# Performance work log

Measured on AMD Instinct MI355X. Metric: run time of the kernel, lower is better.

Reference implementation:

```python
import jax, jax.numpy as jnp
import numpy as np

B, H, L, TAU, THETA = 8192, 256, 4, 8, 8


def setup_inputs() -> dict:
    key = jax.random.key(0)
    ks = jax.random.split(key, 16)
    w = lambda k, shape: (jax.random.normal(k, shape, jnp.float32) * 0.02)
    return {
        "x": jax.random.normal(ks[0], (B, H), jnp.float32),
        "t_att": jax.random.normal(ks[1], (L, TAU, B, H), jnp.float32),
        "s_att": jax.random.normal(ks[2], (L, TAU, B, H), jnp.float32),
        "embed_w": w(ks[3], (H, H)),
        "embed_b": jnp.zeros((H,), jnp.float32),
        "wtn": w(ks[4], (L, H, H)),
        "btn": jnp.zeros((L, H), jnp.float32),
        "wsn": w(ks[5], (L, H, H)),
        "bsn": jnp.zeros((L, H), jnp.float32),
        "wt": w(ks[6], (L, 3 * H, H)),
        "bt": jnp.zeros((L, 3 * H), jnp.float32),
        "ws": w(ks[7], (L, 3 * H, H)),
        "bs": jnp.zeros((L, 3 * H), jnp.float32),
        "out_w": w(ks[8], (H, H)),
        "out_b": jnp.zeros((H,), jnp.float32),
    }


def _forward(x, t_att, s_att, embed_w, embed_b, wtn, btn, wsn, bsn, wt, bt, ws, bs, out_w, out_b):
    n_layers, tau = t_att.shape[0], t_att.shape[1]
    b, h = x.shape
    scale = 1.0 / np.sqrt(h).astype(np.float32)
    theta = THETA

    S = x @ embed_w.T + embed_b  # embed: [B, H]
    # rolling spatial buffers, start as theta zero entries
    t_sp = jnp.zeros((theta, b, h), x.dtype)
    s_sp = jnp.zeros((theta, b, h), x.dtype)

    for i in range(n_layers):
        T_last = t_att[i, -1]  # [B, H]
        # append current S_t / last T_t to spatial buffers, keep last theta
        s_sp = jnp.concatenate([s_sp[1:], S[None]], axis=0)
        t_sp = jnp.concatenate([t_sp[1:], T_last[None]], axis=0)
        # s_att[i].append(S_t); slice last tau -> keys include current S
        s_keys = jnp.concatenate([s_att[i, 1:], S[None]], axis=0)  # [tau, B, H]
        t_vals = t_att[i]  # [tau, B, H]

        s_next = S @ wsn[i].T + bsn[i]
        t_next = T_last @ wtn[i].T + btn[i]

        # temporal attention over last-tau history
        w_t = jax.nn.softmax(jnp.einsum('kbh,bh->kb', s_keys, s_next) * scale, axis=0)
        T_trend = jnp.einsum('kb,kbh->bh', w_t, t_vals)
        t_gate = jax.nn.sigmoid(t_next)
        T_fusion = T_last * t_gate + (1.0 - t_gate) * T_trend

        # spatial attention over last-theta buffer
        w_s = jax.nn.softmax(jnp.einsum('kbh,bh->kb', t_sp, t_next) * scale, axis=0)
        S_trend = jnp.einsum('kb,kbh->bh', w_s, s_sp)
        s_gate = jax.nn.sigmoid(s_next)
        S_fusion = S * s_gate + (1.0 - s_gate) * S_trend

        Tc = T_fusion @ wt[i].T + bt[i]  # [B, 3H]
        Sc = S_fusion @ ws[i].T + bs[i]
        t_g, t_t_, t_s_ = jnp.split(Tc, 3, axis=-1)
        s_g, s_t_, s_s_ = jnp.split(Sc, 3, axis=-1)
        Tg = jax.nn.sigmoid(t_g)
        Sg = jax.nn.sigmoid(s_g)
        # T_new feeds the (stateful) history; S carries to next layer
        S = Sg * s_s_ + (1.0 - Sg) * t_s_

    return jnp.tanh(S @ out_w.T + out_b)


def reference(x, t_att, s_att, embed_w, embed_b, wtn, btn, wsn, bsn, wt, bt, ws, bs, out_w, out_b):
    return _forward(x, t_att, s_att, embed_w, embed_b, wtn, btn, wsn, bsn, wt, bt, ws, bs, out_w, out_b)
```

## Files before the change

kernel.cpp:

```cpp
#include <hip/hip_runtime.h>
#include <cmath>

typedef __attribute__((ext_vector_type(8))) short short8;
typedef __attribute__((ext_vector_type(4))) float f32x4;
typedef __attribute__((ext_vector_type(4))) unsigned short us4;
typedef unsigned short u16;

#define BATCH 8192
#define HDIM  256
static constexpr size_t BH = (size_t)BATCH * HDIM;

__device__ __forceinline__ u16 f2bf(float f) {
    union { float f; unsigned u; } v; v.f = f;
    unsigned r = v.u + 0x7FFFu + ((v.u >> 16) & 1u);
    return (u16)(r >> 16);
}
__device__ __forceinline__ float bf2f(u16 u) {
    union { unsigned u; float f; } v; v.u = ((unsigned)u) << 16;
    return v.f;
}
__device__ __forceinline__ float wred(float v) {
#pragma unroll
    for (int o = 32; o > 0; o >>= 1) v += __shfl_xor(v, o);
    return v;
}
__device__ __forceinline__ float sigmoidf_(float x) {
    return 1.f / (1.f + __expf(-x));
}
__device__ __forceinline__ short8 cvt8(const float* p) {
    f32x4 lo = *(const f32x4*)p, hi = *(const f32x4*)(p + 4);
    short8 t;
    t[0] = (short)f2bf(lo[0]); t[1] = (short)f2bf(lo[1]);
    t[2] = (short)f2bf(lo[2]); t[3] = (short)f2bf(lo[3]);
    t[4] = (short)f2bf(hi[0]); t[5] = (short)f2bf(hi[1]);
    t[6] = (short)f2bf(hi[2]); t[7] = (short)f2bf(hi[3]);
    return t;
}

__global__ __launch_bounds__(256) void convert_weights(
    const float* __restrict__ embed_w, const float* __restrict__ wtn,
    const float* __restrict__ wsn, const float* __restrict__ wt,
    const float* __restrict__ ws, const float* __restrict__ out_w,
    u16* __restrict__ dst)
{
    int idx = blockIdx.x * 256 + threadIdx.x;
    int e = idx * 4;
    if (e >= 22 * 65536) return;
    int c = e >> 16, o = e & 65535;
    const float* src;
    if (c == 0)      src = embed_w + o;
    else if (c < 5)  src = wtn + (size_t)(c - 1) * 65536 + o;
    else if (c < 9)  src = wsn + (size_t)(c - 5) * 65536 + o;
    else if (c < 13) src = wt + (size_t)(c - 9) * 768 * 256 + 512 * 256 + o;
    else if (c < 17) src = ws + (size_t)(c - 13) * 768 * 256 + o;
    else if (c < 21) src = ws + (size_t)(c - 17) * 768 * 256 + 512 * 256 + o;
    else             src = out_w + o;
    f32x4 v = *(const f32x4*)src;
    us4 r;
#pragma unroll
    for (int j = 0; j < 4; ++j) r[j] = f2bf(v[j]);
    *(us4*)(dst + e) = r;
}

#define PAD 264
__global__ __launch_bounds__(512, 4) void stau_mega(
    const float* __restrict__ x,
    const float* __restrict__ t_att, const float* __restrict__ s_att,
    const u16* __restrict__ Wbf,
    const float* __restrict__ embed_b,
    const float* __restrict__ btn, const float* __restrict__ bsn,
    const float* __restrict__ bt, const float* __restrict__ bs,
    const float* __restrict__ out_b,
    float* __restrict__ outp)
{
    __shared__ __align__(16) u16 S_lds[5][16][PAD];
    __shared__ __align__(16) u16 sn_lds[16][PAD];
    __shared__ __align__(16) u16 tn_lds[16][PAD];
    __shared__ __align__(16) u16 tf_lds[16][PAD];
    __shared__ __align__(16) u16 sf_lds[16][PAD];

    const int lane = threadIdx.x & 63;
    const int wave = threadIdx.x >> 6;
    const int lr = lane & 15;
    const int kg = lane >> 4;
    const int row0 = blockIdx.x * 16;
    const float scale = 0.0625f;

    {
        const int n0 = wave * 32;
        f32x4 acc[2] = {};
        for (int k0 = 0; k0 < 256; k0 += 32) {
            int k = k0 + kg * 8;
            short8 a = cvt8(x + (size_t)(row0 + lr) * 256 + k);
#pragma unroll
            for (int nf = 0; nf < 2; ++nf) {
                short8 b = *(const short8*)(Wbf + (size_t)(n0 + nf * 16 + lr) * 256 + k);
                acc[nf] = __builtin_amdgcn_mfma_f32_16x16x32_bf16(a, b, acc[nf], 0, 0, 0);
            }
        }
#pragma unroll
        for (int nf = 0; nf < 2; ++nf) {
            int n = n0 + nf * 16 + lr;
            float bn = embed_b[n];
#pragma unroll
            for (int r = 0; r < 4; ++r)
                S_lds[0][kg * 4 + r][n] = f2bf(acc[nf][r] + bn);
        }
    }
    __syncthreads();

    for (int i = 0; i < 4; ++i) {
        {
            const int g = wave >> 2;
            const int n0 = (wave & 3) * 64;
            const u16* Wm = Wbf + (size_t)((g ? 1 : 5) + i) * 65536;
            const float* bias = (g ? btn : bsn) + i * 256;
            f32x4 acc[4] = {};
            for (int k0 = 0; k0 < 256; k0 += 32) {
                int k = k0 + kg * 8;
                short8 a;
                if (g == 0) a = *(const short8*)(&S_lds[i][lr][k]);
                else        a = cvt8(t_att + ((size_t)i * 8 + 7) * BH + (size_t)(row0 + lr) * 256 + k);
#pragma unroll
                for (int nf = 0; nf < 4; ++nf) {
                    short8 b = *(const short8*)(Wm + (size_t)(n0 + nf * 16 + lr) * 256 + k);
                    acc[nf] = __builtin_amdgcn_mfma_f32_16x16x32_bf16(a, b, acc[nf], 0, 0, 0);
                }
            }
            u16 (*dst)[PAD] = g ? tn_lds : sn_lds;
#pragma unroll
            for (int nf = 0; nf < 4; ++nf) {
                int n = n0 + nf * 16 + lr;
                float bn = bias[n];
#pragma unroll
                for (int r = 0; r < 4; ++r)
                    dst[kg * 4 + r][n] = f2bf(acc[nf][r] + bn);
            }
        }
        __syncthreads();

        for (int rr = wave * 2; rr < wave * 2 + 2; ++rr) {
            const size_t ro = (size_t)(row0 + rr) * 256 + lane * 4;
            const float* sa = s_att + (size_t)i * 8 * BH + ro;
            const float* ta = t_att + (size_t)i * 8 * BH + ro;

            f32x4 sav[7], tav[8], tspv[3];
#pragma unroll
            for (int kk = 0; kk < 7; ++kk) sav[kk] = *(const f32x4*)(sa + (size_t)(kk + 1) * BH);
#pragma unroll
            for (int kk = 0; kk < 8; ++kk) tav[kk] = *(const f32x4*)(ta + (size_t)kk * BH);
#pragma unroll
            for (int jj = 0; jj < 3; ++jj)
                if (jj < i) tspv[jj] = *(const f32x4*)(t_att + ((size_t)jj * 8 + 7) * BH + ro);

            us4 snu = *(const us4*)&sn_lds[rr][lane * 4];
            us4 tnu = *(const us4*)&tn_lds[rr][lane * 4];
            us4 scu = *(const us4*)&S_lds[i][rr][lane * 4];
            float sn[4], tn[4], Sc[4];
#pragma unroll
            for (int j = 0; j < 4; ++j) { sn[j] = bf2f(snu[j]); tn[j] = bf2f(tnu[j]); Sc[j] = bf2f(scu[j]); }

            float lt[8];
#pragma unroll
            for (int kk = 0; kk < 7; ++kk)
                lt[kk] = wred(sav[kk][0] * sn[0] + sav[kk][1] * sn[1] + sav[kk][2] * sn[2] + sav[kk][3] * sn[3]) * scale;
            lt[7] = wred(Sc[0] * sn[0] + Sc[1] * sn[1] + Sc[2] * sn[2] + Sc[3] * sn[3]) * scale;

            float m = lt[0];
#pragma unroll
            for (int kk = 1; kk < 8; ++kk) m = fmaxf(m, lt[kk]);
            float w8[8], den = 0.f;
#pragma unroll
            for (int kk = 0; kk < 8; ++kk) { w8[kk] = __expf(lt[kk] - m); den += w8[kk]; }
            float inv = 1.f / den;

            float Tt[4] = {0.f, 0.f, 0.f, 0.f};
#pragma unroll
            for (int kk = 0; kk < 8; ++kk)
#pragma unroll
                for (int j = 0; j < 4; ++j) Tt[j] += w8[kk] * tav[kk][j];
            us4 ot;
#pragma unroll
            for (int j = 0; j < 4; ++j) {
                float g = sigmoidf_(tn[j]);
                ot[j] = f2bf(tav[7][j] * g + (1.f - g) * Tt[j] * inv);
            }
            *(us4*)&tf_lds[rr][lane * 4] = ot;

            float lsp[4];
#pragma unroll
            for (int jj = 0; jj < 3; ++jj)
                if (jj < i)
                    lsp[jj] = wred(tspv[jj][0] * tn[0] + tspv[jj][1] * tn[1] + tspv[jj][2] * tn[2] + tspv[jj][3] * tn[3]) * scale;
            lsp[3] = wred(tav[7][0] * tn[0] + tav[7][1] * tn[1] + tav[7][2] * tn[2] + tav[7][3] * tn[3]) * scale;

            float ms = fmaxf(0.f, lsp[3]);
#pragma unroll
            for (int jj = 0; jj < 3; ++jj)
                if (jj < i) ms = fmaxf(ms, lsp[jj]);
            float dens = (float)(7 - i) * __expf(-ms);
            float St[4] = {0.f, 0.f, 0.f, 0.f};
#pragma unroll
            for (int jj = 0; jj < 3; ++jj)
                if (jj < i) {
                    float w = __expf(lsp[jj] - ms);
                    dens += w;
                    us4 shu = *(const us4*)&S_lds[jj][rr][lane * 4];
#pragma unroll
                    for (int j = 0; j < 4; ++j) St[j] += w * bf2f(shu[j]);
                }
            {
                float w = __expf(lsp[3] - ms);
                dens += w;
#pragma unroll
                for (int j = 0; j < 4; ++j) St[j] += w * Sc[j];
            }
            float invs = 1.f / dens;
            us4 os;
#pragma unroll
            for (int j = 0; j < 4; ++j) {
                float g = sigmoidf_(sn[j]);
                os[j] = f2bf(Sc[j] * g + (1.f - g) * St[j] * invs);
            }
            *(us4*)&sf_lds[rr][lane * 4] = os;
        }
        __syncthreads();

        {
            const int n0 = wave * 32;
            const u16* Wt3 = Wbf + (size_t)(9  + i) * 65536;
            const u16* Ws1 = Wbf + (size_t)(13 + i) * 65536;
            const u16* Ws3 = Wbf + (size_t)(17 + i) * 65536;
            f32x4 aT[2] = {}, aG[2] = {}, aS[2] = {};
            for (int k0 = 0; k0 < 256; k0 += 32) {
                int k = k0 + kg * 8;
                short8 at = *(const short8*)(&tf_lds[lr][k]);
                short8 as = *(const short8*)(&sf_lds[lr][k]);
#pragma unroll
                for (int nf = 0; nf < 2; ++nf) {
                    size_t wo = (size_t)(n0 + nf * 16 + lr) * 256 + k;
                    aT[nf] = __builtin_amdgcn_mfma_f32_16x16x32_bf16(at, *(const short8*)(Wt3 + wo), aT[nf], 0, 0, 0);
                    aG[nf] = __builtin_amdgcn_mfma_f32_16x16x32_bf16(as, *(const short8*)(Ws1 + wo), aG[nf], 0, 0, 0);
                    aS[nf] = __builtin_amdgcn_mfma_f32_16x16x32_bf16(as, *(const short8*)(Ws3 + wo), aS[nf], 0, 0, 0);
                }
            }
            const float* b1 = bt + i * 768 + 512;
            const float* b2 = bs + i * 768;
            const float* b3 = bs + i * 768 + 512;
#pragma unroll
            for (int nf = 0; nf < 2; ++nf) {
                int n = n0 + nf * 16 + lr;
                float bb1 = b1[n], bb2 = b2[n], bb3 = b3[n];
#pragma unroll
                for (int r = 0; r < 4; ++r) {
                    float gv = sigmoidf_(aG[nf][r] + bb2);
                    float v = gv * (aS[nf][r] + bb3) + (1.f - gv) * (aT[nf][r] + bb1);
                    S_lds[i + 1][kg * 4 + r][n] = f2bf(v);
                }
            }
        }
        __syncthreads();
    }

    {
        const int n0 = wave * 32;
        const u16* Wo = Wbf + (size_t)21 * 65536;
        f32x4 acc[2] = {};
        for (int k0 = 0; k0 < 256; k0 += 32) {
            int k = k0 + kg * 8;
            short8 a = *(const short8*)(&S_lds[4][lr][k]);
#pragma unroll
            for (int nf = 0; nf < 2; ++nf) {
                short8 b = *(const short8*)(Wo + (size_t)(n0 + nf * 16 + lr) * 256 + k);
                acc[nf] = __builtin_amdgcn_mfma_f32_16x16x32_bf16(a, b, acc[nf], 0, 0, 0);
            }
        }
#pragma unroll
        for (int nf = 0; nf < 2; ++nf) {
            int n = n0 + nf * 16 + lr;
            float bn = out_b[n];
#pragma unroll
            for (int r = 0; r < 4; ++r)
                outp[(size_t)(row0 + kg * 4 + r) * 256 + n] = tanhf(acc[nf][r] + bn);
        }
    }
}

extern "C" void kernel_launch(void* const* d_in, const int* in_sizes, int n_in,
                              void* d_out, int out_size, void* d_ws, size_t ws_size,
                              hipStream_t stream)
{
    (void)in_sizes; (void)n_in; (void)out_size; (void)ws_size;
    const float* x       = (const float*)d_in[0];
    const float* t_att   = (const float*)d_in[1];
    const float* s_att   = (const float*)d_in[2];
    const float* embed_w = (const float*)d_in[3];
    const float* embed_b = (const float*)d_in[4];
    const float* wtn     = (const float*)d_in[5];
    const float* btn     = (const float*)d_in[6];
    const float* wsn     = (const float*)d_in[7];
    const float* bsn     = (const float*)d_in[8];
    const float* wt      = (const float*)d_in[9];
    const float* bt      = (const float*)d_in[10];
    const float* ws_in   = (const float*)d_in[11];
    const float* bs      = (const float*)d_in[12];
    const float* out_w   = (const float*)d_in[13];
    const float* out_b   = (const float*)d_in[14];

    u16* Wbf = (u16*)d_ws;

    convert_weights<<<1408, 256, 0, stream>>>(embed_w, wtn, wsn, wt, ws_in, out_w, Wbf);

    stau_mega<<<BATCH / 16, 512, 0, stream>>>(
        x, t_att, s_att, Wbf, embed_b, btn, bsn, bt, bs, out_b, (float*)d_out);
}
```

Before: 305.7 us.

## Split fused megakernel into per-stage GEMM and templated attention kernels

Replaces the single fused per-block kernel with separate launches: an embed GEMM, and then for each layer a dual GEMM, a layer-templated attention kernel and a triple GEMM, followed by an output GEMM. Intermediates now go through global workspace in bf16 instead of LDS. The attention kernel batches all wave reductions into one interleaved shuffle loop and issues loads early, which is meant to raise memory-level parallelism and occupancy. The cost is extra global traffic for intermediates and about 14 kernel launches in place of one.

```diff
diff --git a/kernel.cpp b/kernel.cpp
--- a/kernel.cpp
+++ b/kernel.cpp
@@ -18,11 +18,6 @@
 __device__ __forceinline__ float bf2f(u16 u) {
     union { unsigned u; float f; } v; v.u = ((unsigned)u) << 16;
     return v.f;
-}
-__device__ __forceinline__ float wred(float v) {
-#pragma unroll
-    for (int o = 32; o > 0; o >>= 1) v += __shfl_xor(v, o);
-    return v;
 }
 __device__ __forceinline__ float sigmoidf_(float x) {
     return 1.f / (1.f + __expf(-x));
@@ -35,6 +30,9 @@
     t[4] = (short)f2bf(hi[0]); t[5] = (short)f2bf(hi[1]);
     t[6] = (short)f2bf(hi[2]); t[7] = (short)f2bf(hi[3]);
     return t;
+}
+__device__ __forceinline__ float dot4(const f32x4& a, const float* b) {
+    return a[0] * b[0] + a[1] * b[1] + a[2] * b[2] + a[3] * b[3];
 }
 
 __global__ __launch_bounds__(256) void convert_weights(
@@ -62,228 +60,235 @@
     *(us4*)(dst + e) = r;
 }
 
-#define PAD 264
-__global__ __launch_bounds__(512, 4) void stau_mega(
-    const float* __restrict__ x,
+__global__ __launch_bounds__(512, 4) void gemm_embed(
+    const float* __restrict__ x, const u16* __restrict__ W,
+    const float* __restrict__ bias, u16* __restrict__ S0)
+{
+    const int lane = threadIdx.x & 63, wave = threadIdx.x >> 6;
+    const int lr = lane & 15, kg = lane >> 4;
+    const int row0 = blockIdx.x * 16;
+    const int n0 = wave * 32;
+    f32x4 acc[2] = {};
+    for (int k0 = 0; k0 < 256; k0 += 32) {
+        int k = k0 + kg * 8;
+        short8 a = cvt8(x + (size_t)(row0 + lr) * 256 + k);
+#pragma unroll
+        for (int nf = 0; nf < 2; ++nf) {
+            short8 b = *(const short8*)(W + (size_t)(n0 + nf * 16 + lr) * 256 + k);
+            acc[nf] = __builtin_amdgcn_mfma_f32_16x16x32_bf16(a, b, acc[nf], 0, 0, 0);
+        }
+    }
+#pragma unroll
+    for (int nf = 0; nf < 2; ++nf) {
+        int n = n0 + nf * 16 + lr;
+        float bn = bias[n];
+#pragma unroll
+        for (int r = 0; r < 4; ++r)
+            S0[(size_t)(row0 + kg * 4 + r) * 256 + n] = f2bf(acc[nf][r] + bn);
+    }
+}
+
+__global__ __launch_bounds__(512, 4) void gemm_out(
+    const u16* __restrict__ S4, const u16* __restrict__ W,
+    const float* __restrict__ bias, float* __restrict__ outp)
+{
+    const int lane = threadIdx.x & 63, wave = threadIdx.x >> 6;
+    const int lr = lane & 15, kg = lane >> 4;
+    const int row0 = blockIdx.x * 16;
+    const int n0 = wave * 32;
+    f32x4 acc[2] = {};
+    for (int k0 = 0; k0 < 256; k0 += 32) {
+        int k = k0 + kg * 8;
+        short8 a = *(const short8*)(S4 + (size_t)(row0 + lr) * 256 + k);
+#pragma unroll
+        for (int nf = 0; nf < 2; ++nf) {
+            short8 b = *(const short8*)(W + (size_t)(n0 + nf * 16 + lr) * 256 + k);
+            acc[nf] = __builtin_amdgcn_mfma_f32_16x16x32_bf16(a, b, acc[nf], 0, 0, 0);
+        }
+    }
+#pragma unroll
+    for (int nf = 0; nf < 2; ++nf) {
+        int n = n0 + nf * 16 + lr;
+        float bn = bias[n];
+#pragma unroll
+        for (int r = 0; r < 4; ++r)
+            outp[(size_t)(row0 + kg * 4 + r) * 256 + n] = tanhf(acc[nf][r] + bn);
+    }
+}
+
+__global__ __launch_bounds__(512, 4) void gemm_dual(
+    const u16* __restrict__ Scur, const float* __restrict__ Tlast,
+    const u16* __restrict__ Wsn, const u16* __restrict__ Wtn,
+    const float* __restrict__ bsn_l, const float* __restrict__ btn_l,
+    u16* __restrict__ sn_g, u16* __restrict__ tn_g)
+{
+    const int lane = threadIdx.x & 63, wave = threadIdx.x >> 6;
+    const int lr = lane & 15, kg = lane >> 4;
+    const int row0 = blockIdx.x * 16;
+    const int g = wave >> 2;
+    const int n0 = (wave & 3) * 64;
+    const u16* Wm = g ? Wtn : Wsn;
+    f32x4 acc[4] = {};
+    for (int k0 = 0; k0 < 256; k0 += 32) {
+        int k = k0 + kg * 8;
+        short8 a;
+        if (g == 0) a = *(const short8*)(Scur + (size_t)(row0 + lr) * 256 + k);
+        else        a = cvt8(Tlast + (size_t)(row0 + lr) * 256 + k);
+#pragma unroll
+        for (int nf = 0; nf < 4; ++nf) {
+            short8 b = *(const short8*)(Wm + (size_t)(n0 + nf * 16 + lr) * 256 + k);
+            acc[nf] = __builtin_amdgcn_mfma_f32_16x16x32_bf16(a, b, acc[nf], 0, 0, 0);
+        }
+    }
+    const float* bias = g ? btn_l : bsn_l;
+    u16* dst = g ? tn_g : sn_g;
+#pragma unroll
+    for (int nf = 0; nf < 4; ++nf) {
+        int n = n0 + nf * 16 + lr;
+        float bn = bias[n];
+#pragma unroll
+        for (int r = 0; r < 4; ++r)
+            dst[(size_t)(row0 + kg * 4 + r) * 256 + n] = f2bf(acc[nf][r] + bn);
+    }
+}
+
+__global__ __launch_bounds__(512, 4) void gemm_triple(
+    const u16* __restrict__ Tf, const u16* __restrict__ Sf,
+    const u16* __restrict__ Wt3, const u16* __restrict__ Ws1, const u16* __restrict__ Ws3,
+    const float* __restrict__ b1p, const float* __restrict__ b2p, const float* __restrict__ b3p,
+    u16* __restrict__ Sout)
+{
+    const int lane = threadIdx.x & 63, wave = threadIdx.x >> 6;
+    const int lr = lane & 15, kg = lane >> 4;
+    const int row0 = blockIdx.x * 16;
+    const int n0 = wave * 32;
+    f32x4 aT[2] = {}, aG[2] = {}, aS[2] = {};
+    for (int k0 = 0; k0 < 256; k0 += 32) {
+        int k = k0 + kg * 8;
+        short8 at = *(const short8*)(Tf + (size_t)(row0 + lr) * 256 + k);
+        short8 as = *(const short8*)(Sf + (size_t)(row0 + lr) * 256 + k);
+#pragma unroll
+        for (int nf = 0; nf < 2; ++nf) {
+            size_t wo = (size_t)(n0 + nf * 16 + lr) * 256 + k;
+            aT[nf] = __builtin_amdgcn_mfma_f32_16x16x32_bf16(at, *(const short8*)(Wt3 + wo), aT[nf], 0, 0, 0);
+            aG[nf] = __builtin_amdgcn_mfma_f32_16x16x32_bf16(as, *(const short8*)(Ws1 + wo), aG[nf], 0, 0, 0);
+            aS[nf] = __builtin_amdgcn_mfma_f32_16x16x32_bf16(as, *(const short8*)(Ws3 + wo), aS[nf], 0, 0, 0);
+        }
+    }
+#pragma unroll
+    for (int nf = 0; nf < 2; ++nf) {
+        int n = n0 + nf * 16 + lr;
+        float bb1 = b1p[n], bb2 = b2p[n], bb3 = b3p[n];
+#pragma unroll
+        for (int r = 0; r < 4; ++r) {
+            float gv = sigmoidf_(aG[nf][r] + bb2);
+            float v = gv * (aS[nf][r] + bb3) + (1.f - gv) * (aT[nf][r] + bb1);
+            Sout[(size_t)(row0 + kg * 4 + r) * 256 + n] = f2bf(v);
+        }
+    }
+}
+
+template<int LAYER>
+__global__ __launch_bounds__(256, 4) void attn_k(
     const float* __restrict__ t_att, const float* __restrict__ s_att,
-    const u16* __restrict__ Wbf,
-    const float* __restrict__ embed_b,
-    const float* __restrict__ btn, const float* __restrict__ bsn,
-    const float* __restrict__ bt, const float* __restrict__ bs,
-    const float* __restrict__ out_b,
-    float* __restrict__ outp)
-{
-    __shared__ __align__(16) u16 S_lds[5][16][PAD];
-    __shared__ __align__(16) u16 sn_lds[16][PAD];
-    __shared__ __align__(16) u16 tn_lds[16][PAD];
-    __shared__ __align__(16) u16 tf_lds[16][PAD];
-    __shared__ __align__(16) u16 sf_lds[16][PAD];
-
+    const u16* __restrict__ S_hist,
+    const u16* __restrict__ sn_g, const u16* __restrict__ tn_g,
+    u16* __restrict__ tf_g, u16* __restrict__ sf_g)
+{
     const int lane = threadIdx.x & 63;
-    const int wave = threadIdx.x >> 6;
-    const int lr = lane & 15;
-    const int kg = lane >> 4;
-    const int row0 = blockIdx.x * 16;
+    const int row = blockIdx.x * 4 + (threadIdx.x >> 6);
+    const size_t ro = (size_t)row * 256 + lane * 4;
     const float scale = 0.0625f;
 
+    const float* sa = s_att + (size_t)LAYER * 8 * BH + ro;
+    const float* ta = t_att + (size_t)LAYER * 8 * BH + ro;
+
+    f32x4 sav[7];
+#pragma unroll
+    for (int kk = 0; kk < 7; ++kk) sav[kk] = *(const f32x4*)(sa + (size_t)(kk + 1) * BH);
+    f32x4 tav7 = *(const f32x4*)(ta + (size_t)7 * BH);
+    f32x4 tspv[LAYER > 0 ? LAYER : 1];
+    us4 shu[LAYER > 0 ? LAYER : 1];
+#pragma unroll
+    for (int jj = 0; jj < LAYER; ++jj) {
+        tspv[jj] = *(const f32x4*)(t_att + ((size_t)jj * 8 + 7) * BH + ro);
+        shu[jj]  = *(const us4*)(S_hist + (size_t)jj * BH + ro);
+    }
+    us4 scu = *(const us4*)(S_hist + (size_t)LAYER * BH + ro);
+    us4 snu = *(const us4*)(sn_g + ro);
+    us4 tnu = *(const us4*)(tn_g + ro);
+
+    float sn[4], tn[4], Sc[4];
+#pragma unroll
+    for (int j = 0; j < 4; ++j) { sn[j] = bf2f(snu[j]); tn[j] = bf2f(tnu[j]); Sc[j] = bf2f(scu[j]); }
+
+    constexpr int NV = 9 + LAYER;
+    float v[NV];
+#pragma unroll
+    for (int kk = 0; kk < 7; ++kk) v[kk] = dot4(sav[kk], sn);
+    v[7] = Sc[0] * sn[0] + Sc[1] * sn[1] + Sc[2] * sn[2] + Sc[3] * sn[3];
+#pragma unroll
+    for (int jj = 0; jj < LAYER; ++jj) v[8 + jj] = dot4(tspv[jj], tn);
+    v[8 + LAYER] = dot4(tav7, tn);
+
+    f32x4 tav[7];
+#pragma unroll
+    for (int kk = 0; kk < 7; ++kk) tav[kk] = *(const f32x4*)(ta + (size_t)kk * BH);
+
+#pragma unroll
+    for (int o = 32; o > 0; o >>= 1)
+#pragma unroll
+        for (int u = 0; u < NV; ++u) v[u] += __shfl_xor(v[u], o);
+
+    float m = v[0] * scale;
+#pragma unroll
+    for (int kk = 1; kk < 8; ++kk) m = fmaxf(m, v[kk] * scale);
+    float w8[8], den = 0.f;
+#pragma unroll
+    for (int kk = 0; kk < 8; ++kk) { w8[kk] = __expf(v[kk] * scale - m); den += w8[kk]; }
+    float inv = 1.f / den;
+
+    float Tt[4];
+#pragma unroll
+    for (int j = 0; j < 4; ++j) Tt[j] = w8[7] * tav7[j];
+#pragma unroll
+    for (int kk = 0; kk < 7; ++kk)
+#pragma unroll
+        for (int j = 0; j < 4; ++j) Tt[j] += w8[kk] * tav[kk][j];
+    us4 ot;
+#pragma unroll
+    for (int j = 0; j < 4; ++j) {
+        float g = sigmoidf_(tn[j]);
+        ot[j] = f2bf(tav7[j] * g + (1.f - g) * Tt[j] * inv);
+    }
+    *(us4*)(tf_g + ro) = ot;
+
+    float ms = fmaxf(0.f, v[8 + LAYER] * scale);
+#pragma unroll
+    for (int jj = 0; jj < LAYER; ++jj) ms = fmaxf(ms, v[8 + jj] * scale);
+    float dens = (float)(7 - LAYER) * __expf(-ms);
+    float St[4];
     {
-        const int n0 = wave * 32;
-        f32x4 acc[2] = {};
-        for (int k0 = 0; k0 < 256; k0 += 32) {
-            int k = k0 + kg * 8;
-            short8 a = cvt8(x + (size_t)(row0 + lr) * 256 + k);
-#pragma unroll
-            for (int nf = 0; nf < 2; ++nf) {
-                short8 b = *(const short8*)(Wbf + (size_t)(n0 + nf * 16 + lr) * 256 + k);
-                acc[nf] = __builtin_amdgcn_mfma_f32_16x16x32_bf16(a, b, acc[nf], 0, 0, 0);
-            }
-        }
-#pragma unroll
-        for (int nf = 0; nf < 2; ++nf) {
-            int n = n0 + nf * 16 + lr;
-            float bn = embed_b[n];
-#pragma unroll
-            for (int r = 0; r < 4; ++r)
-                S_lds[0][kg * 4 + r][n] = f2bf(acc[nf][r] + bn);
-        }
-    }
-    __syncthreads();
-
-    for (int i = 0; i < 4; ++i) {
-        {
-            const int g = wave >> 2;
-            const int n0 = (wave & 3) * 64;
-            const u16* Wm = Wbf + (size_t)((g ? 1 : 5) + i) * 65536;
-            const float* bias = (g ? btn : bsn) + i * 256;
-            f32x4 acc[4] = {};
-            for (int k0 = 0; k0 < 256; k0 += 32) {
-                int k = k0 + kg * 8;
-                short8 a;
-                if (g == 0) a = *(const short8*)(&S_lds[i][lr][k]);
-                else        a = cvt8(t_att + ((size_t)i * 8 + 7) * BH + (size_t)(row0 + lr) * 256 + k);
-#pragma unroll
-                for (int nf = 0; nf < 4; ++nf) {
-                    short8 b = *(const short8*)(Wm + (size_t)(n0 + nf * 16 + lr) * 256 + k);
-                    acc[nf] = __builtin_amdgcn_mfma_f32_16x16x32_bf16(a, b, acc[nf], 0, 0, 0);
-                }
-            }
-            u16 (*dst)[PAD] = g ? tn_lds : sn_lds;
-#pragma unroll
-            for (int nf = 0; nf < 4; ++nf) {
-                int n = n0 + nf * 16 + lr;
-                float bn = bias[n];
-#pragma unroll
-                for (int r = 0; r < 4; ++r)
-                    dst[kg * 4 + r][n] = f2bf(acc[nf][r] + bn);
-            }
-        }
-        __syncthreads();
-
-        for (int rr = wave * 2; rr < wave * 2 + 2; ++rr) {
-            const size_t ro = (size_t)(row0 + rr) * 256 + lane * 4;
-            const float* sa = s_att + (size_t)i * 8 * BH + ro;
-            const float* ta = t_att + (size_t)i * 8 * BH + ro;
-
-            f32x4 sav[7], tav[8], tspv[3];
-#pragma unroll
-            for (int kk = 0; kk < 7; ++kk) sav[kk] = *(const f32x4*)(sa + (size_t)(kk + 1) * BH);
-#pragma unroll
-            for (int kk = 0; kk < 8; ++kk) tav[kk] = *(const f32x4*)(ta + (size_t)kk * BH);
-#pragma unroll
-            for (int jj = 0; jj < 3; ++jj)
-                if (jj < i) tspv[jj] = *(const f32x4*)(t_att + ((size_t)jj * 8 + 7) * BH + ro);
-
-            us4 snu = *(const us4*)&sn_lds[rr][lane * 4];
-            us4 tnu = *(const us4*)&tn_lds[rr][lane * 4];
-            us4 scu = *(const us4*)&S_lds[i][rr][lane * 4];
-            float sn[4], tn[4], Sc[4];
-#pragma unroll
-            for (int j = 0; j < 4; ++j) { sn[j] = bf2f(snu[j]); tn[j] = bf2f(tnu[j]); Sc[j] = bf2f(scu[j]); }
-
-            float lt[8];
-#pragma unroll
-            for (int kk = 0; kk < 7; ++kk)
-                lt[kk] = wred(sav[kk][0] * sn[0] + sav[kk][1] * sn[1] + sav[kk][2] * sn[2] + sav[kk][3] * sn[3]) * scale;
-            lt[7] = wred(Sc[0] * sn[0] + Sc[1] * sn[1] + Sc[2] * sn[2] + Sc[3] * sn[3]) * scale;
-
-            float m = lt[0];
-#pragma unroll
-            for (int kk = 1; kk < 8; ++kk) m = fmaxf(m, lt[kk]);
-            float w8[8], den = 0.f;
-#pragma unroll
-            for (int kk = 0; kk < 8; ++kk) { w8[kk] = __expf(lt[kk] - m); den += w8[kk]; }
-            float inv = 1.f / den;
-
-            float Tt[4] = {0.f, 0.f, 0.f, 0.f};
-#pragma unroll
-            for (int kk = 0; kk < 8; ++kk)
-#pragma unroll
-                for (int j = 0; j < 4; ++j) Tt[j] += w8[kk] * tav[kk][j];
-            us4 ot;
-#pragma unroll
-            for (int j = 0; j < 4; ++j) {
-                float g = sigmoidf_(tn[j]);
-                ot[j] = f2bf(tav[7][j] * g + (1.f - g) * Tt[j] * inv);
-            }
-            *(us4*)&tf_lds[rr][lane * 4] = ot;
-
-            float lsp[4];
-#pragma unroll
-            for (int jj = 0; jj < 3; ++jj)
-                if (jj < i)
-                    lsp[jj] = wred(tspv[jj][0] * tn[0] + tspv[jj][1] * tn[1] + tspv[jj][2] * tn[2] + tspv[jj][3] * tn[3]) * scale;
-            lsp[3] = wred(tav[7][0] * tn[0] + tav[7][1] * tn[1] + tav[7][2] * tn[2] + tav[7][3] * tn[3]) * scale;
-
-            float ms = fmaxf(0.f, lsp[3]);
-#pragma unroll
-            for (int jj = 0; jj < 3; ++jj)
-                if (jj < i) ms = fmaxf(ms, lsp[jj]);
-            float dens = (float)(7 - i) * __expf(-ms);
-            float St[4] = {0.f, 0.f, 0.f, 0.f};
-#pragma unroll
-            for (int jj = 0; jj < 3; ++jj)
-                if (jj < i) {
-                    float w = __expf(lsp[jj] - ms);
-                    dens += w;
-                    us4 shu = *(const us4*)&S_lds[jj][rr][lane * 4];
-#pragma unroll
-                    for (int j = 0; j < 4; ++j) St[j] += w * bf2f(shu[j]);
-                }
-            {
-                float w = __expf(lsp[3] - ms);
-                dens += w;
-#pragma unroll
-                for (int j = 0; j < 4; ++j) St[j] += w * Sc[j];
-            }
-            float invs = 1.f / dens;
-            us4 os;
-#pragma unroll
-            for (int j = 0; j < 4; ++j) {
-                float g = sigmoidf_(sn[j]);
-                os[j] = f2bf(Sc[j] * g + (1.f - g) * St[j] * invs);
-            }
-            *(us4*)&sf_lds[rr][lane * 4] = os;
-        }
-        __syncthreads();
-
-        {
-            const int n0 = wave * 32;
-            const u16* Wt3 = Wbf + (size_t)(9  + i) * 65536;
-            const u16* Ws1 = Wbf + (size_t)(13 + i) * 65536;
-            const u16* Ws3 = Wbf + (size_t)(17 + i) * 65536;
-            f32x4 aT[2] = {}, aG[2] = {}, aS[2] = {};
-            for (int k0 = 0; k0 < 256; k0 += 32) {
-                int k = k0 + kg * 8;
-                short8 at = *(const short8*)(&tf_lds[lr][k]);
-                short8 as = *(const short8*)(&sf_lds[lr][k]);
-#pragma unroll
-                for (int nf = 0; nf < 2; ++nf) {
-                    size_t wo = (size_t)(n0 + nf * 16 + lr) * 256 + k;
-                    aT[nf] = __builtin_amdgcn_mfma_f32_16x16x32_bf16(at, *(const short8*)(Wt3 + wo), aT[nf], 0, 0, 0);
-                    aG[nf] = __builtin_amdgcn_mfma_f32_16x16x32_bf16(as, *(const short8*)(Ws1 + wo), aG[nf], 0, 0, 0);
-                    aS[nf] = __builtin_amdgcn_mfma_f32_16x16x32_bf16(as, *(const short8*)(Ws3 + wo), aS[nf], 0, 0, 0);
-                }
-            }
-            const float* b1 = bt + i * 768 + 512;
-            const float* b2 = bs + i * 768;
-            const float* b3 = bs + i * 768 + 512;
-#pragma unroll
-            for (int nf = 0; nf < 2; ++nf) {
-                int n = n0 + nf * 16 + lr;
-                float bb1 = b1[n], bb2 = b2[n], bb3 = b3[n];
-#pragma unroll
-                for (int r = 0; r < 4; ++r) {
-                    float gv = sigmoidf_(aG[nf][r] + bb2);
-                    float v = gv * (aS[nf][r] + bb3) + (1.f - gv) * (aT[nf][r] + bb1);
-                    S_lds[i + 1][kg * 4 + r][n] = f2bf(v);
-                }
-            }
-        }
-        __syncthreads();
-    }
-
-    {
-        const int n0 = wave * 32;
-        const u16* Wo = Wbf + (size_t)21 * 65536;
-        f32x4 acc[2] = {};
-        for (int k0 = 0; k0 < 256; k0 += 32) {
-            int k = k0 + kg * 8;
-            short8 a = *(const short8*)(&S_lds[4][lr][k]);
-#pragma unroll
-            for (int nf = 0; nf < 2; ++nf) {
-                short8 b = *(const short8*)(Wo + (size_t)(n0 + nf * 16 + lr) * 256 + k);
-                acc[nf] = __builtin_amdgcn_mfma_f32_16x16x32_bf16(a, b, acc[nf], 0, 0, 0);
-            }
-        }
-#pragma unroll
-        for (int nf = 0; nf < 2; ++nf) {
-            int n = n0 + nf * 16 + lr;
-            float bn = out_b[n];
-#pragma unroll
-            for (int r = 0; r < 4; ++r)
-                outp[(size_t)(row0 + kg * 4 + r) * 256 + n] = tanhf(acc[nf][r] + bn);
-        }
-    }
+        float w = __expf(v[8 + LAYER] * scale - ms);
+        dens += w;
+#pragma unroll
+        for (int j = 0; j < 4; ++j) St[j] = w * Sc[j];
+    }
+#pragma unroll
+    for (int jj = 0; jj < LAYER; ++jj) {
+        float w = __expf(v[8 + jj] * scale - ms);
+        dens += w;
+#pragma unroll
+        for (int j = 0; j < 4; ++j) St[j] += w * bf2f(shu[jj][j]);
+    }
+    float invs = 1.f / dens;
+    us4 os;
+#pragma unroll
+    for (int j = 0; j < 4; ++j) {
+        float g = sigmoidf_(sn[j]);
+        os[j] = f2bf(Sc[j] * g + (1.f - g) * St[j] * invs);
+    }
+    *(us4*)(sf_g + ro) = os;
 }
 
 extern "C" void kernel_launch(void* const* d_in, const int* in_sizes, int n_in,
@@ -307,10 +312,40 @@
     const float* out_w   = (const float*)d_in[13];
     const float* out_b   = (const float*)d_in[14];
 
-    u16* Wbf = (u16*)d_ws;
+    u16* wsp    = (u16*)d_ws;
+    u16* Wbf    = wsp;
+    u16* S_hist = wsp + (size_t)22 * 65536;
+    u16* sn_g   = S_hist + 5 * BH;
+    u16* tn_g   = sn_g + BH;
+    u16* tf_g   = tn_g + BH;
+    u16* sf_g   = tf_g + BH;
 
     convert_weights<<<1408, 256, 0, stream>>>(embed_w, wtn, wsn, wt, ws_in, out_w, Wbf);
 
-    stau_mega<<<BATCH / 16, 512, 0, stream>>>(
-        x, t_att, s_att, Wbf, embed_b, btn, bsn, bt, bs, out_b, (float*)d_out);
-}
+    gemm_embed<<<BATCH / 16, 512, 0, stream>>>(x, Wbf, embed_b, S_hist);
+
+    for (int i = 0; i < 4; ++i) {
+        gemm_dual<<<BATCH / 16, 512, 0, stream>>>(
+            S_hist + (size_t)i * BH, t_att + ((size_t)i * 8 + 7) * BH,
+            Wbf + (size_t)(5 + i) * 65536, Wbf + (size_t)(1 + i) * 65536,
+            bsn + i * 256, btn + i * 256, sn_g, tn_g);
+
+        switch (i) {
+            case 0: attn_k<0><<<BATCH / 4, 256, 0, stream>>>(t_att, s_att, S_hist, sn_g, tn_g, tf_g, sf_g); break;
+            case 1: attn_k<1><<<BATCH / 4, 256, 0, stream>>>(t_att, s_att, S_hist, sn_g, tn_g, tf_g, sf_g); break;
+            case 2: attn_k<2><<<BATCH / 4, 256, 0, stream>>>(t_att, s_att, S_hist, sn_g, tn_g, tf_g, sf_g); break;
+            case 3: attn_k<3><<<BATCH / 4, 256, 0, stream>>>(t_att, s_att, S_hist, sn_g, tn_g, tf_g, sf_g); break;
+        }
+
+        gemm_triple<<<BATCH / 16, 512, 0, stream>>>(
+            tf_g, sf_g,
+            Wbf + (size_t)(9 + i) * 65536,
+            Wbf + (size_t)(13 + i) * 65536,
+            Wbf + (size_t)(17 + i) * 65536,
+            bt + i * 768 + 512, bs + i * 768, bs + i * 768 + 512,
+            S_hist + (size_t)(i + 1) * BH);
+    }
+
+    gemm_out<<<BATCH / 16, 512, 0, stream>>>(
+        S_hist + (size_t)4 * BH, Wbf + (size_t)21 * 65536, out_b, (float*)d_out);
+}
```

New measurement: 379.1 us. +24.0%, slower.

## Halve block size to 4 waves and batch attention-score wave reductions

Applied to the files above, without the earlier changes.

Blocks shrink from 8 waves to 4. Each wave now computes twice as many output column tiles in every GEMM stage and handles four rows in the attention stage. The twelve attention dot products (temporal and spatial) are also reduced together in one interleaved butterfly shuffle loop, replacing twelve separate reductions, which gives more instruction-level parallelism. The goal is less per-wave overhead and better latency hiding, but each wave holds more accumulator and load registers and the block has fewer waves available to hide memory latency.

```diff
diff --git a/kernel.cpp b/kernel.cpp
--- a/kernel.cpp
+++ b/kernel.cpp
@@ -18,11 +18,6 @@
 __device__ __forceinline__ float bf2f(u16 u) {
     union { unsigned u; float f; } v; v.u = ((unsigned)u) << 16;
     return v.f;
-}
-__device__ __forceinline__ float wred(float v) {
-#pragma unroll
-    for (int o = 32; o > 0; o >>= 1) v += __shfl_xor(v, o);
-    return v;
 }
 __device__ __forceinline__ float sigmoidf_(float x) {
     return 1.f / (1.f + __expf(-x));
@@ -35,6 +30,9 @@
     t[4] = (short)f2bf(hi[0]); t[5] = (short)f2bf(hi[1]);
     t[6] = (short)f2bf(hi[2]); t[7] = (short)f2bf(hi[3]);
     return t;
+}
+__device__ __forceinline__ float dot4(const f32x4& a, const float* b) {
+    return a[0] * b[0] + a[1] * b[1] + a[2] * b[2] + a[3] * b[3];
 }
 
 __global__ __launch_bounds__(256) void convert_weights(
@@ -63,7 +61,7 @@
 }
 
 #define PAD 264
-__global__ __launch_bounds__(512, 4) void stau_mega(
+__global__ __launch_bounds__(256, 2) void stau_mega(
     const float* __restrict__ x,
     const float* __restrict__ t_att, const float* __restrict__ s_att,
     const u16* __restrict__ Wbf,
@@ -87,19 +85,19 @@
     const float scale = 0.0625f;
 
     {
-        const int n0 = wave * 32;
-        f32x4 acc[2] = {};
+        const int n0 = wave * 64;
+        f32x4 acc[4] = {};
         for (int k0 = 0; k0 < 256; k0 += 32) {
             int k = k0 + kg * 8;
             short8 a = cvt8(x + (size_t)(row0 + lr) * 256 + k);
 #pragma unroll
-            for (int nf = 0; nf < 2; ++nf) {
+            for (int nf = 0; nf < 4; ++nf) {
                 short8 b = *(const short8*)(Wbf + (size_t)(n0 + nf * 16 + lr) * 256 + k);
                 acc[nf] = __builtin_amdgcn_mfma_f32_16x16x32_bf16(a, b, acc[nf], 0, 0, 0);
             }
         }
 #pragma unroll
-        for (int nf = 0; nf < 2; ++nf) {
+        for (int nf = 0; nf < 4; ++nf) {
             int n = n0 + nf * 16 + lr;
             float bn = embed_b[n];
 #pragma unroll
@@ -111,25 +109,25 @@
 
     for (int i = 0; i < 4; ++i) {
         {
-            const int g = wave >> 2;
-            const int n0 = (wave & 3) * 64;
+            const int g = wave >> 1;
+            const int n0 = (wave & 1) * 128;
             const u16* Wm = Wbf + (size_t)((g ? 1 : 5) + i) * 65536;
             const float* bias = (g ? btn : bsn) + i * 256;
-            f32x4 acc[4] = {};
+            f32x4 acc[8] = {};
             for (int k0 = 0; k0 < 256; k0 += 32) {
                 int k = k0 + kg * 8;
                 short8 a;
                 if (g == 0) a = *(const short8*)(&S_lds[i][lr][k]);
                 else        a = cvt8(t_att + ((size_t)i * 8 + 7) * BH + (size_t)(row0 + lr) * 256 + k);
 #pragma unroll
-                for (int nf = 0; nf < 4; ++nf) {
+                for (int nf = 0; nf < 8; ++nf) {
                     short8 b = *(const short8*)(Wm + (size_t)(n0 + nf * 16 + lr) * 256 + k);
                     acc[nf] = __builtin_amdgcn_mfma_f32_16x16x32_bf16(a, b, acc[nf], 0, 0, 0);
                 }
             }
             u16 (*dst)[PAD] = g ? tn_lds : sn_lds;
 #pragma unroll
-            for (int nf = 0; nf < 4; ++nf) {
+            for (int nf = 0; nf < 8; ++nf) {
                 int n = n0 + nf * 16 + lr;
                 float bn = bias[n];
 #pragma unroll
@@ -139,12 +137,12 @@
         }
         __syncthreads();
 
-        for (int rr = wave * 2; rr < wave * 2 + 2; ++rr) {
+        for (int rr = wave * 4; rr < wave * 4 + 4; ++rr) {
             const size_t ro = (size_t)(row0 + rr) * 256 + lane * 4;
             const float* sa = s_att + (size_t)i * 8 * BH + ro;
             const float* ta = t_att + (size_t)i * 8 * BH + ro;
 
-            f32x4 sav[7], tav[8], tspv[3];
+            f32x4 sav[7], tav[8], tspv[3] = {};
 #pragma unroll
             for (int kk = 0; kk < 7; ++kk) sav[kk] = *(const f32x4*)(sa + (size_t)(kk + 1) * BH);
 #pragma unroll
@@ -160,18 +158,25 @@
 #pragma unroll
             for (int j = 0; j < 4; ++j) { sn[j] = bf2f(snu[j]); tn[j] = bf2f(tnu[j]); Sc[j] = bf2f(scu[j]); }
 
-            float lt[8];
-#pragma unroll
-            for (int kk = 0; kk < 7; ++kk)
-                lt[kk] = wred(sav[kk][0] * sn[0] + sav[kk][1] * sn[1] + sav[kk][2] * sn[2] + sav[kk][3] * sn[3]) * scale;
-            lt[7] = wred(Sc[0] * sn[0] + Sc[1] * sn[1] + Sc[2] * sn[2] + Sc[3] * sn[3]) * scale;
-
-            float m = lt[0];
-#pragma unroll
-            for (int kk = 1; kk < 8; ++kk) m = fmaxf(m, lt[kk]);
+            float v[12];
+#pragma unroll
+            for (int kk = 0; kk < 7; ++kk) v[kk] = dot4(sav[kk], sn);
+            v[7] = Sc[0] * sn[0] + Sc[1] * sn[1] + Sc[2] * sn[2] + Sc[3] * sn[3];
+#pragma unroll
+            for (int jj = 0; jj < 3; ++jj) v[8 + jj] = (jj < i) ? dot4(tspv[jj], tn) : 0.f;
+            v[11] = dot4(tav[7], tn);
+
+#pragma unroll
+            for (int o = 32; o > 0; o >>= 1)
+#pragma unroll
+                for (int u = 0; u < 12; ++u) v[u] += __shfl_xor(v[u], o);
+
+            float m = v[0] * scale;
+#pragma unroll
+            for (int kk = 1; kk < 8; ++kk) m = fmaxf(m, v[kk] * scale);
             float w8[8], den = 0.f;
 #pragma unroll
-            for (int kk = 0; kk < 8; ++kk) { w8[kk] = __expf(lt[kk] - m); den += w8[kk]; }
+            for (int kk = 0; kk < 8; ++kk) { w8[kk] = __expf(v[kk] * scale - m); den += w8[kk]; }
             float inv = 1.f / den;
 
             float Tt[4] = {0.f, 0.f, 0.f, 0.f};
@@ -187,34 +192,27 @@
             }
             *(us4*)&tf_lds[rr][lane * 4] = ot;
 
-            float lsp[4];
+            float ms = fmaxf(0.f, v[11] * scale);
 #pragma unroll
             for (int jj = 0; jj < 3; ++jj)
-                if (jj < i)
-                    lsp[jj] = wred(tspv[jj][0] * tn[0] + tspv[jj][1] * tn[1] + tspv[jj][2] * tn[2] + tspv[jj][3] * tn[3]) * scale;
-            lsp[3] = wred(tav[7][0] * tn[0] + tav[7][1] * tn[1] + tav[7][2] * tn[2] + tav[7][3] * tn[3]) * scale;
-
-            float ms = fmaxf(0.f, lsp[3]);
-#pragma unroll
-            for (int jj = 0; jj < 3; ++jj)
-                if (jj < i) ms = fmaxf(ms, lsp[jj]);
+                if (jj < i) ms = fmaxf(ms, v[8 + jj] * scale);
             float dens = (float)(7 - i) * __expf(-ms);
-            float St[4] = {0.f, 0.f, 0.f, 0.f};
+            float St[4];
+            {
+                float w = __expf(v[11] * scale - ms);
+                dens += w;
+#pragma unroll
+                for (int j = 0; j < 4; ++j) St[j] = w * Sc[j];
+            }
 #pragma unroll
             for (int jj = 0; jj < 3; ++jj)
                 if (jj < i) {
-                    float w = __expf(lsp[jj] - ms);
+                    float w = __expf(v[8 + jj] * scale - ms);
                     dens += w;
                     us4 shu = *(const us4*)&S_lds[jj][rr][lane * 4];
 #pragma unroll
                     for (int j = 0; j < 4; ++j) St[j] += w * bf2f(shu[j]);
                 }
-            {
-                float w = __expf(lsp[3] - ms);
-                dens += w;
-#pragma unroll
-                for (int j = 0; j < 4; ++j) St[j] += w * Sc[j];
-            }
             float invs = 1.f / dens;
             us4 os;
 #pragma unroll
@@ -227,17 +225,17 @@
         __syncthreads();
 
         {
-            const int n0 = wave * 32;
+            const int n0 = wave * 64;
             const u16* Wt3 = Wbf + (size_t)(9  + i) * 65536;
             const u16* Ws1 = Wbf + (size_t)(13 + i) * 65536;
             const u16* Ws3 = Wbf + (size_t)(17 + i) * 65536;
-            f32x4 aT[2] = {}, aG[2] = {}, aS[2] = {};
+            f32x4 aT[4] = {}, aG[4] = {}, aS[4] = {};
             for (int k0 = 0; k0 < 256; k0 += 32) {
                 int k = k0 + kg * 8;
                 short8 at = *(const short8*)(&tf_lds[lr][k]);
                 short8 as = *(const short8*)(&sf_lds[lr][k]);
 #pragma unroll
-                for (int nf = 0; nf < 2; ++nf) {
+                for (int nf = 0; nf < 4; ++nf) {
                     size_t wo = (size_t)(n0 + nf * 16 + lr) * 256 + k;
                     aT[nf] = __builtin_amdgcn_mfma_f32_16x16x32_bf16(at, *(const short8*)(Wt3 + wo), aT[nf], 0, 0, 0);
                     aG[nf] = __builtin_amdgcn_mfma_f32_16x16x32_bf16(as, *(const short8*)(Ws1 + wo), aG[nf], 0, 0, 0);
@@ -248,14 +246,14 @@
             const float* b2 = bs + i * 768;
             const float* b3 = bs + i * 768 + 512;
 #pragma unroll
-            for (int nf = 0; nf < 2; ++nf) {
+            for (int nf = 0; nf < 4; ++nf) {
                 int n = n0 + nf * 16 + lr;
                 float bb1 = b1[n], bb2 = b2[n], bb3 = b3[n];
 #pragma unroll
                 for (int r = 0; r < 4; ++r) {
                     float gv = sigmoidf_(aG[nf][r] + bb2);
-                    float v = gv * (aS[nf][r] + bb3) + (1.f - gv) * (aT[nf][r] + bb1);
-                    S_lds[i + 1][kg * 4 + r][n] = f2bf(v);
+                    float vv = gv * (aS[nf][r] + bb3) + (1.f - gv) * (aT[nf][r] + bb1);
+                    S_lds[i + 1][kg * 4 + r][n] = f2bf(vv);
                 }
             }
         }
@@ -263,20 +261,20 @@
     }
 
     {
-        const int n0 = wave * 32;
+        const int n0 = wave * 64;
         const u16* Wo = Wbf + (size_t)21 * 65536;
-        f32x4 acc[2] = {};
+        f32x4 acc[4] = {};
         for (int k0 = 0; k0 < 256; k0 += 32) {
             int k = k0 + kg * 8;
             short8 a = *(const short8*)(&S_lds[4][lr][k]);
 #pragma unroll
-            for (int nf = 0; nf < 2; ++nf) {
+            for (int nf = 0; nf < 4; ++nf) {
                 short8 b = *(const short8*)(Wo + (size_t)(n0 + nf * 16 + lr) * 256 + k);
                 acc[nf] = __builtin_amdgcn_mfma_f32_16x16x32_bf16(a, b, acc[nf], 0, 0, 0);
             }
         }
 #pragma unroll
-        for (int nf = 0; nf < 2; ++nf) {
+        for (int nf = 0; nf < 4; ++nf) {
             int n = n0 + nf * 16 + lr;
             float bn = out_b[n];
 #pragma unroll
@@ -311,6 +309,6 @@
 
     convert_weights<<<1408, 256, 0, stream>>>(embed_w, wtn, wsn, wt, ws_in, out_w, Wbf);
 
-    stau_mega<<<BATCH / 16, 512, 0, stream>>>(
+    stau_mega<<<BATCH / 16, 256, 0, stream>>>(
         x, t_att, s_att, Wbf, embed_b, btn, bsn, bt, bs, out_b, (float*)d_out);
 }
```

New measurement: 278.3 us. 1.1x faster.
